# Kernel tuning notes

Measured on AMD Instinct MI355X. Metric: run time of the kernel, lower is better.

The kernel has to match this reference:

```python
import jax, jax.numpy as jnp
import numpy as np

N_NODES = 50000
N_EDGES = 800000
D_IN = 512
D_OUT = 256


def setup_inputs() -> dict:
    key = jax.random.key(0)
    k1, k2, k3 = jax.random.split(key, 3)
    x = jax.random.normal(k1, (N_NODES, D_IN), dtype=jnp.float32)
    edge_index = jax.random.randint(k2, (2, N_EDGES), 0, N_NODES, dtype=jnp.int64)
    # Glorot-style init for the GCN weight, zero bias (PyG defaults)
    W = jax.random.normal(k3, (D_IN, D_OUT), dtype=jnp.float32) * (1.0 / np.sqrt(D_IN))
    b = jnp.zeros((D_OUT,), dtype=jnp.float32)
    return {"x": x, "edge_index": edge_index, "W": W, "b": b}


def reference(x, edge_index, W, b):
    N = x.shape[0]
    # 1) dense linear transform (the compute-heavy GEMM)
    xw = x @ W  # [N, d_out]

    # 2) add self-loops (PyG GCNConv default)
    loop = jnp.arange(N, dtype=edge_index.dtype)
    row = jnp.concatenate([edge_index[0], loop])  # sources
    col = jnp.concatenate([edge_index[1], loop])  # targets

    # 3) symmetric normalization deg^{-1/2} on targets (in-degree incl. self-loops)
    deg = jax.ops.segment_sum(jnp.ones_like(col, dtype=xw.dtype), col, num_segments=N)
    dinv = jnp.where(deg > 0, jax.lax.rsqrt(deg), 0.0)
    norm = dinv[row] * dinv[col]  # [E+N]

    # 4) gather source features, scale, scatter-add to targets
    msgs = xw[row] * norm[:, None]  # [E+N, d_out]
    agg = jax.ops.segment_sum(msgs, col, num_segments=N)  # [N, d_out]

    # 5) bias + ReLU (dropout is identity in eval mode)
    return jax.nn.relu(agg + b)
```

## Files before the change

kernel.cpp:

```cpp
#include <hip/hip_runtime.h>
#include <hip/hip_bf16.h>

#define N_NODES 50000
#define N_EDGES 800000
#define D_IN    512
#define D_OUT   256
#define NBLK_SCAN ((N_NODES + 1023) / 1024)
#define GEMM_NWG (((N_NODES + 127) / 128) * 2)
#define GEMM_Q   (GEMM_NWG / 8)
#define GEMM_R   (GEMM_NWG % 8)
#define FILL_NB  260
#define FUSE_NB  (GEMM_NWG + FILL_NB)
#define GATH_CHUNKS ((N_NODES + 63) / 64)

typedef short s8v  __attribute__((ext_vector_type(8)));
typedef float f32x4 __attribute__((ext_vector_type(4)));

__device__ __forceinline__ unsigned short bf16b(float f) {
    __hip_bfloat16 h = __float2bfloat16(f);
    return *reinterpret_cast<unsigned short*>(&h);
}
__device__ __forceinline__ float bflo(unsigned u) { return __uint_as_float(u << 16); }
__device__ __forceinline__ float bfhi(unsigned u) { return __uint_as_float(u & 0xffff0000u); }

#define GLD16(gp, lp)                                                           \
    __builtin_amdgcn_global_load_lds(                                           \
        (const __attribute__((address_space(1))) unsigned int*)(const void*)(gp),\
        (__attribute__((address_space(3))) unsigned int*)(void*)(lp), 16, 0, 0)

__device__ __forceinline__ int wave_incl_scan(int v, int lane) {
    #pragma unroll
    for (int d = 1; d < 64; d <<= 1) {
        int u = __shfl_up(v, d, 64);
        if (lane >= d) v += u;
    }
    return v;
}

__global__ void k_wt(const float* __restrict__ W, unsigned short* __restrict__ Wt,
                     int* __restrict__ cnt4) {
    int k = blockIdx.x;
    int n = threadIdx.x;
    Wt[(size_t)n * D_IN + k] = bf16b(W[(size_t)k * D_OUT + n]);
    int t = (blockIdx.x * 256 + threadIdx.x) * 2;
    if (t < 4 * N_NODES) {
        cnt4[t] = 0;
        if (t + 1 < 4 * N_NODES) cnt4[t + 1] = 0;
    }
}


__global__ void k_count(const int* __restrict__ col, int* __restrict__ cnt4) {
    int i = (blockIdx.x * 256 + threadIdx.x) * 2;
    if (i < N_EDGES) {
        int2 c = *(const int2*)&col[i];
        atomicAdd(&cnt4[(i & 3) * N_NODES + c.x], 1);
        atomicAdd(&cnt4[((i + 1) & 3) * N_NODES + c.y], 1);
    }
}

__launch_bounds__(256)
__global__ void k_scan1(const int* __restrict__ cnt4, int* __restrict__ bsum) {
    const int t = threadIdx.x, b = blockIdx.x;
    const int idx = b * 1024 + t * 4;
    int s = 0;
    if (idx < N_NODES) {
        #pragma unroll
        for (int q = 0; q < 4; ++q) {
            int4 v = *(const int4*)&cnt4[q * N_NODES + idx];
            s += (v.x + v.y) + (v.z + v.w);
        }
    }
    #pragma unroll
    for (int d = 1; d < 64; d <<= 1) s += __shfl_xor(s, d, 64);
    __shared__ int ws[4];
    if ((t & 63) == 0) ws[t >> 6] = s;
    __syncthreads();
    if (t == 0) bsum[b] = ws[0] + ws[1] + ws[2] + ws[3];
}

__launch_bounds__(256)
__global__ void k_scan3(const int* __restrict__ cnt4, const int* __restrict__ bsum,
                        int* __restrict__ row_ptr, float* __restrict__ dinv,
                        int* __restrict__ cursor4) {
    const int t = threadIdx.x, b = blockIdx.x;
    const int lane = t & 63, wv = t >> 6;
    const int idx = b * 1024 + t * 4;
    int4 vq[4];
    int4 tot = make_int4(0, 0, 0, 0);
    if (idx < N_NODES) {
        #pragma unroll
        for (int q = 0; q < 4; ++q) {
            vq[q] = *(const int4*)&cnt4[q * N_NODES + idx];
            tot.x += vq[q].x; tot.y += vq[q].y;
            tot.z += vq[q].z; tot.w += vq[q].w;
        }
    } else {
        #pragma unroll
        for (int q = 0; q < 4; ++q) vq[q] = make_int4(0, 0, 0, 0);
    }
    int s = (tot.x + tot.y) + (tot.z + tot.w);
    int isc = wave_incl_scan(s, lane);
    __shared__ int wsum[4];
    __shared__ int s_boff;
    if (lane == 63) wsum[wv] = isc;
    if (t < 64) {
        int u = (t < b) ? bsum[t] : 0;
        #pragma unroll
        for (int d = 1; d < 64; d <<= 1) u += __shfl_xor(u, d, 64);
        if (t == 0) s_boff = u;
    }
    __syncthreads();
    int off = s_boff;
    #pragma unroll
    for (int i = 0; i < 4; ++i)
        if (i < wv) off += wsum[i];
    int p0 = off + isc - s;
    int p1 = p0 + tot.x;
    int p2 = p1 + tot.y;
    int p3 = p2 + tot.z;
    if (idx < N_NODES) {
        row_ptr[idx + 0] = p0; dinv[idx + 0] = rsqrtf(1.f + (float)tot.x);
        row_ptr[idx + 1] = p1; dinv[idx + 1] = rsqrtf(1.f + (float)tot.y);
        row_ptr[idx + 2] = p2; dinv[idx + 2] = rsqrtf(1.f + (float)tot.z);
        row_ptr[idx + 3] = p3; dinv[idx + 3] = rsqrtf(1.f + (float)tot.w);
        int4 run = make_int4(p0, p1, p2, p3);
        #pragma unroll
        for (int q = 0; q < 4; ++q) {
            *(int4*)&cursor4[q * N_NODES + idx] = run;
            run.x += vq[q].x; run.y += vq[q].y;
            run.z += vq[q].z; run.w += vq[q].w;
        }
    }
    if (b == 0 && t == 0) row_ptr[N_NODES] = N_EDGES;
}

__launch_bounds__(256)
__global__ void k_gemm(const float* __restrict__ A,
                       const unsigned short* __restrict__ Wt,
                       const float* __restrict__ dinv,
                       unsigned short* __restrict__ yb,
                       const int* __restrict__ row, const int* __restrict__ col,
                       int* __restrict__ cursor4, int* __restrict__ csr_src)
{
    __shared__ __align__(16) float          As[128 * 64];
    __shared__ __align__(16) unsigned short Bs[128 * 64];

    const int bid = blockIdx.x;
    const int t   = threadIdx.x;

    if ((bid & 3) == 3) {
        const int cid = bid >> 2;
        const int stride = FILL_NB * 256 * 2;
        for (int i = (cid * 256 + t) * 2; i < N_EDGES; i += stride) {
            int2 c = *(const int2*)&col[i];
            int2 r = *(const int2*)&row[i];
            int p0 = atomicAdd(&cursor4[(i & 3) * N_NODES + c.x], 1);
            csr_src[p0] = r.x;
            int p1 = atomicAdd(&cursor4[((i + 1) & 3) * N_NODES + c.y], 1);
            csr_src[p1] = r.y;
        }
        return;
    }

    const int gid = bid - (bid >> 2);

    int xcd = gid % 8, pos = gid / 8;
    int wg = (xcd < GEMM_R) ? xcd * (GEMM_Q + 1) + pos
                            : GEMM_R * (GEMM_Q + 1) + (xcd - GEMM_R) * GEMM_Q + pos;
    const int nt = wg & 1;
    const int mt = wg >> 1;
    const int m0 = mt * 128;
    const int n0 = nt * 128;

    const int w  = t >> 6;
    const int l  = t & 63;
    const int wm = (w >> 1) * 64;
    const int wn = (w & 1) * 64;
    const int lr = l & 15;
    const int lk = l >> 4;

    size_t aoff[8];
    #pragma unroll
    for (int i = 0; i < 8; ++i) {
        int rw = m0 + w * 32 + i * 4 + (l >> 4);
        if (rw >= N_NODES) rw = 0;
        int sslot = (l & 15) ^ (rw & 7);
        aoff[i] = (size_t)rw * D_IN + sslot * 4;
    }
    const int srow = l >> 3;
    const int srcj = (l & 7) ^ srow;
    size_t boff[4];
    #pragma unroll
    for (int i = 0; i < 4; ++i) {
        int g = w * 4 + i;
        int bn = n0 + g * 8 + srow;
        boff[i] = (size_t)bn * D_IN + srcj * 8;
    }

    f32x4 acc[4][4] = {};

    for (int kk = 0; kk < D_IN; kk += 64) {
        #pragma unroll
        for (int i = 0; i < 8; ++i)
            GLD16(&A[aoff[i] + kk], (char*)As + (w * 32 + i * 4) * 256);
        #pragma unroll
        for (int i = 0; i < 4; ++i)
            GLD16(&Wt[boff[i] + kk], (char*)Bs + (w * 4 + i) * 1024);
        __syncthreads();

        #pragma unroll
        for (int ks = 0; ks < 2; ++ks) {
            s8v af[4], bfr[4];
            #pragma unroll
            for (int f = 0; f < 4; ++f) {
                int rw = wm + f * 16 + lr;
                int a  = (ks * 4 + lk) * 2;
                int s0 = a ^ (lr & 7);
                int s1 = (a + 1) ^ (lr & 7);
                const char* pr = (const char*)As + rw * 256;
                float4 x0 = *(const float4*)(pr + s0 * 16);
                float4 x1 = *(const float4*)(pr + s1 * 16);
                union { s8v v; unsigned short h[8]; } u;
                u.h[0] = bf16b(x0.x); u.h[1] = bf16b(x0.y);
                u.h[2] = bf16b(x0.z); u.h[3] = bf16b(x0.w);
                u.h[4] = bf16b(x1.x); u.h[5] = bf16b(x1.y);
                u.h[6] = bf16b(x1.z); u.h[7] = bf16b(x1.w);
                af[f] = u.v;
            }
            const int kb = (ks * 64 + lk * 16) ^ ((lr & 7) << 4);
            #pragma unroll
            for (int f = 0; f < 4; ++f)
                bfr[f] = *(const s8v*)((const char*)Bs + ((wn + f * 16 + lr) * 128 + kb));
            #pragma unroll
            for (int fm = 0; fm < 4; ++fm)
                #pragma unroll
                for (int fn = 0; fn < 4; ++fn)
                    acc[fm][fn] = __builtin_amdgcn_mfma_f32_16x16x32_bf16(
                        af[fm], bfr[fn], acc[fm][fn], 0, 0, 0);
        }
        __syncthreads();
    }

    #pragma unroll
    for (int fm = 0; fm < 4; ++fm) {
        #pragma unroll
        for (int j = 0; j < 4; ++j) {
            int rw = m0 + wm + fm * 16 + lk * 4 + j;
            if (rw < N_NODES) {
                float s = dinv[rw];
                #pragma unroll
                for (int fn = 0; fn < 4; ++fn) {
                    int cl = n0 + wn + fn * 16 + lr;
                    size_t off = (size_t)(cl >> 5) * (N_NODES * 32)
                               + (size_t)rw * 32 + (cl & 31);
                    yb[off] = bf16b(acc[fm][fn][j] * s);
                }
            }
        }
    }
}

__device__ __forceinline__ void add8(float* acc, uint4 q) {
    unsigned x;
    x = q.x; acc[0] += bflo(x); acc[1] += bfhi(x);
    x = q.y; acc[2] += bflo(x); acc[3] += bfhi(x);
    x = q.z; acc[4] += bflo(x); acc[5] += bfhi(x);
    x = q.w; acc[6] += bflo(x); acc[7] += bfhi(x);
}

__launch_bounds__(256)
__global__ void k_gather(const int* __restrict__ row_ptr, const int* __restrict__ csr_src,
                         const unsigned short* __restrict__ yb,
                         const float* __restrict__ dinv,
                         const float* __restrict__ bias, float* __restrict__ out)
{
    const int s     = blockIdx.x & 7;
    const int chunk = blockIdx.x >> 3;
    const int g     = threadIdx.x >> 2;
    const int cs    = threadIdx.x & 3;
    const int c     = chunk * 64 + g;
    if (c >= N_NODES) return;

    const uint4* t4 = (const uint4*)(yb + (size_t)s * N_NODES * 32);

    float acc[8] = {0.f,0.f,0.f,0.f,0.f,0.f,0.f,0.f};

    const int e0 = row_ptr[c];
    const int e1 = row_ptr[c + 1];
    for (int i = e0; i < e1; i += 8) {
        int idx[8];
        #pragma unroll
        for (int j = 0; j < 8; ++j) {
            int p = i + j;
            idx[j] = csr_src[p < e1 ? p : e1 - 1];
        }
        uint4 v[8];
        #pragma unroll
        for (int j = 0; j < 8; ++j) v[j] = t4[(size_t)idx[j] * 4 + cs];
        #pragma unroll
        for (int j = 0; j < 8; ++j)
            if (i + j < e1) add8(acc, v[j]);
    }

    add8(acc, t4[(size_t)c * 4 + cs]);

    const float sc = dinv[c];
    const int colb = s * 32 + cs * 8;
    float4 b0 = *(const float4*)&bias[colb];
    float4 b1 = *(const float4*)&bias[colb + 4];
    float4 o0, o1;
    o0.x = fmaxf(fmaf(acc[0], sc, b0.x), 0.f);
    o0.y = fmaxf(fmaf(acc[1], sc, b0.y), 0.f);
    o0.z = fmaxf(fmaf(acc[2], sc, b0.z), 0.f);
    o0.w = fmaxf(fmaf(acc[3], sc, b0.w), 0.f);
    o1.x = fmaxf(fmaf(acc[4], sc, b1.x), 0.f);
    o1.y = fmaxf(fmaf(acc[5], sc, b1.y), 0.f);
    o1.z = fmaxf(fmaf(acc[6], sc, b1.z), 0.f);
    o1.w = fmaxf(fmaf(acc[7], sc, b1.w), 0.f);
    float* dst = &out[(size_t)c * D_OUT + colb];
    *(float4*)dst       = o0;
    *(float4*)(dst + 4) = o1;
}

extern "C" void kernel_launch(void* const* d_in, const int* in_sizes, int n_in,
                              void* d_out, int out_size, void* d_ws, size_t ws_size,
                              hipStream_t stream) {
    const float* x   = (const float*)d_in[0];
    const int*   ei  = (const int*)d_in[1];
    const float* W   = (const float*)d_in[2];
    const float* b   = (const float*)d_in[3];
    float*       out = (float*)d_out;

    const int* row = ei;
    const int* col = ei + N_EDGES;

    char* p = (char*)d_ws;
    unsigned short* yb = (unsigned short*)p;  p += (size_t)N_NODES * D_OUT * 2;
    unsigned short* Wt = (unsigned short*)p;  p += (size_t)D_OUT * D_IN * 2;
    int*   csr_src = (int*)p;                 p += (size_t)N_EDGES * 4;
    int*   cnt4    = (int*)p;                 p += (size_t)4 * N_NODES * 4;
    int*   row_ptr = (int*)p;                 p += (size_t)(N_NODES + 4) * 4;
    int*   cursor4 = (int*)p;                 p += (size_t)4 * N_NODES * 4;
    float* dinv    = (float*)p;               p += (size_t)N_NODES * 4;
    int*   bsum    = (int*)p;                 p += (size_t)NBLK_SCAN * 4;

    k_wt   <<<D_IN, D_OUT, 0, stream>>>(W, Wt, cnt4);
    k_count<<<(N_EDGES / 2 + 255) / 256, 256, 0, stream>>>(col, cnt4);
    k_scan1<<<NBLK_SCAN, 256, 0, stream>>>(cnt4, bsum);
    k_scan3<<<NBLK_SCAN, 256, 0, stream>>>(cnt4, bsum, row_ptr, dinv, cursor4);

    k_gemm<<<FUSE_NB, 256, 0, stream>>>(x, Wt, dinv, yb, row, col, cursor4, csr_src);

    k_gather<<<GATH_CHUNKS * 8, 256, 0, stream>>>(row_ptr, csr_src, yb, dinv, b, out);
}
```

Baseline: 187.7 us.

## Split CSR fill out of GEMM, widen atomic counter banks to eight, merge transpose with count

```diff
diff --git a/kernel.cpp b/kernel.cpp
--- a/kernel.cpp
+++ b/kernel.cpp
@@ -9,9 +9,9 @@
 #define GEMM_NWG (((N_NODES + 127) / 128) * 2)
 #define GEMM_Q   (GEMM_NWG / 8)
 #define GEMM_R   (GEMM_NWG % 8)
-#define FILL_NB  260
-#define FUSE_NB  (GEMM_NWG + FILL_NB)
 #define GATH_CHUNKS ((N_NODES + 63) / 64)
+#define WT_NB    512
+#define CNT_NB   1563
 
 typedef short s8v  __attribute__((ext_vector_type(8)));
 typedef float f32x4 __attribute__((ext_vector_type(4)));
@@ -37,37 +37,34 @@
     return v;
 }
 
-__global__ void k_wt(const float* __restrict__ W, unsigned short* __restrict__ Wt,
-                     int* __restrict__ cnt4) {
-    int k = blockIdx.x;
-    int n = threadIdx.x;
-    Wt[(size_t)n * D_IN + k] = bf16b(W[(size_t)k * D_OUT + n]);
-    int t = (blockIdx.x * 256 + threadIdx.x) * 2;
-    if (t < 4 * N_NODES) {
-        cnt4[t] = 0;
-        if (t + 1 < 4 * N_NODES) cnt4[t + 1] = 0;
-    }
-}
-
-
-__global__ void k_count(const int* __restrict__ col, int* __restrict__ cnt4) {
-    int i = (blockIdx.x * 256 + threadIdx.x) * 2;
+__global__ void k_wtcnt(const float* __restrict__ W, unsigned short* __restrict__ Wt,
+                        const int* __restrict__ col, int* __restrict__ cnt8) {
+    const int bid = blockIdx.x;
+    const int t   = threadIdx.x;
+    if (bid < WT_NB) {
+        int k = bid;
+        int n = t;
+        Wt[(size_t)n * D_IN + k] = bf16b(W[(size_t)k * D_OUT + n]);
+        return;
+    }
+    const int cid = bid - WT_NB;
+    int i = (cid * 256 + t) * 2;
     if (i < N_EDGES) {
         int2 c = *(const int2*)&col[i];
-        atomicAdd(&cnt4[(i & 3) * N_NODES + c.x], 1);
-        atomicAdd(&cnt4[((i + 1) & 3) * N_NODES + c.y], 1);
+        atomicAdd(&cnt8[(i & 7) * N_NODES + c.x], 1);
+        atomicAdd(&cnt8[((i + 1) & 7) * N_NODES + c.y], 1);
     }
 }
 
 __launch_bounds__(256)
-__global__ void k_scan1(const int* __restrict__ cnt4, int* __restrict__ bsum) {
+__global__ void k_scan1(const int* __restrict__ cnt8, int* __restrict__ bsum) {
     const int t = threadIdx.x, b = blockIdx.x;
     const int idx = b * 1024 + t * 4;
     int s = 0;
     if (idx < N_NODES) {
         #pragma unroll
-        for (int q = 0; q < 4; ++q) {
-            int4 v = *(const int4*)&cnt4[q * N_NODES + idx];
+        for (int q = 0; q < 8; ++q) {
+            int4 v = *(const int4*)&cnt8[q * N_NODES + idx];
             s += (v.x + v.y) + (v.z + v.w);
         }
     }
@@ -80,24 +77,24 @@
 }
 
 __launch_bounds__(256)
-__global__ void k_scan3(const int* __restrict__ cnt4, const int* __restrict__ bsum,
+__global__ void k_scan3(const int* __restrict__ cnt8, const int* __restrict__ bsum,
                         int* __restrict__ row_ptr, float* __restrict__ dinv,
-                        int* __restrict__ cursor4) {
+                        int* __restrict__ cursor8) {
     const int t = threadIdx.x, b = blockIdx.x;
     const int lane = t & 63, wv = t >> 6;
     const int idx = b * 1024 + t * 4;
-    int4 vq[4];
+    int4 vq[8];
     int4 tot = make_int4(0, 0, 0, 0);
     if (idx < N_NODES) {
         #pragma unroll
-        for (int q = 0; q < 4; ++q) {
-            vq[q] = *(const int4*)&cnt4[q * N_NODES + idx];
+        for (int q = 0; q < 8; ++q) {
+            vq[q] = *(const int4*)&cnt8[q * N_NODES + idx];
             tot.x += vq[q].x; tot.y += vq[q].y;
             tot.z += vq[q].z; tot.w += vq[q].w;
         }
     } else {
         #pragma unroll
-        for (int q = 0; q < 4; ++q) vq[q] = make_int4(0, 0, 0, 0);
+        for (int q = 0; q < 8; ++q) vq[q] = make_int4(0, 0, 0, 0);
     }
     int s = (tot.x + tot.y) + (tot.z + tot.w);
     int isc = wave_incl_scan(s, lane);
@@ -126,46 +123,39 @@
         row_ptr[idx + 3] = p3; dinv[idx + 3] = rsqrtf(1.f + (float)tot.w);
         int4 run = make_int4(p0, p1, p2, p3);
         #pragma unroll
-        for (int q = 0; q < 4; ++q) {
-            *(int4*)&cursor4[q * N_NODES + idx] = run;
+        for (int q = 0; q < 8; ++q) {
+            *(int4*)&cursor8[q * N_NODES + idx] = run;
             run.x += vq[q].x; run.y += vq[q].y;
             run.z += vq[q].z; run.w += vq[q].w;
         }
     }
     if (b == 0 && t == 0) row_ptr[N_NODES] = N_EDGES;
+}
+
+__global__ void k_fill(const int* __restrict__ row, const int* __restrict__ col,
+                       int* __restrict__ cursor8, int* __restrict__ csr_src) {
+    int i = (blockIdx.x * 256 + threadIdx.x) * 2;
+    if (i < N_EDGES) {
+        int2 c = *(const int2*)&col[i];
+        int2 r = *(const int2*)&row[i];
+        int p0 = atomicAdd(&cursor8[(i & 7) * N_NODES + c.x], 1);
+        csr_src[p0] = r.x;
+        int p1 = atomicAdd(&cursor8[((i + 1) & 7) * N_NODES + c.y], 1);
+        csr_src[p1] = r.y;
+    }
 }
 
 __launch_bounds__(256)
 __global__ void k_gemm(const float* __restrict__ A,
                        const unsigned short* __restrict__ Wt,
                        const float* __restrict__ dinv,
-                       unsigned short* __restrict__ yb,
-                       const int* __restrict__ row, const int* __restrict__ col,
-                       int* __restrict__ cursor4, int* __restrict__ csr_src)
+                       unsigned short* __restrict__ yb)
 {
     __shared__ __align__(16) float          As[128 * 64];
     __shared__ __align__(16) unsigned short Bs[128 * 64];
 
-    const int bid = blockIdx.x;
-    const int t   = threadIdx.x;
-
-    if ((bid & 3) == 3) {
-        const int cid = bid >> 2;
-        const int stride = FILL_NB * 256 * 2;
-        for (int i = (cid * 256 + t) * 2; i < N_EDGES; i += stride) {
-            int2 c = *(const int2*)&col[i];
-            int2 r = *(const int2*)&row[i];
-            int p0 = atomicAdd(&cursor4[(i & 3) * N_NODES + c.x], 1);
-            csr_src[p0] = r.x;
-            int p1 = atomicAdd(&cursor4[((i + 1) & 3) * N_NODES + c.y], 1);
-            csr_src[p1] = r.y;
-        }
-        return;
-    }
-
-    const int gid = bid - (bid >> 2);
-
-    int xcd = gid % 8, pos = gid / 8;
+    int orig = blockIdx.x;
+    int xcd = orig % 8, pos = orig / 8;
     int wg = (xcd < GEMM_R) ? xcd * (GEMM_Q + 1) + pos
                             : GEMM_R * (GEMM_Q + 1) + (xcd - GEMM_R) * GEMM_Q + pos;
     const int nt = wg & 1;
@@ -173,6 +163,7 @@
     const int m0 = mt * 128;
     const int n0 = nt * 128;
 
+    const int t  = threadIdx.x;
     const int w  = t >> 6;
     const int l  = t & 63;
     const int wm = (w >> 1) * 64;
@@ -339,18 +330,19 @@
     unsigned short* yb = (unsigned short*)p;  p += (size_t)N_NODES * D_OUT * 2;
     unsigned short* Wt = (unsigned short*)p;  p += (size_t)D_OUT * D_IN * 2;
     int*   csr_src = (int*)p;                 p += (size_t)N_EDGES * 4;
-    int*   cnt4    = (int*)p;                 p += (size_t)4 * N_NODES * 4;
+    int*   cnt8    = (int*)p;                 p += (size_t)8 * N_NODES * 4;
     int*   row_ptr = (int*)p;                 p += (size_t)(N_NODES + 4) * 4;
-    int*   cursor4 = (int*)p;                 p += (size_t)4 * N_NODES * 4;
+    int*   cursor8 = (int*)p;                 p += (size_t)8 * N_NODES * 4;
     float* dinv    = (float*)p;               p += (size_t)N_NODES * 4;
     int*   bsum    = (int*)p;                 p += (size_t)NBLK_SCAN * 4;
 
-    k_wt   <<<D_IN, D_OUT, 0, stream>>>(W, Wt, cnt4);
-    k_count<<<(N_EDGES / 2 + 255) / 256, 256, 0, stream>>>(col, cnt4);
-    k_scan1<<<NBLK_SCAN, 256, 0, stream>>>(cnt4, bsum);
-    k_scan3<<<NBLK_SCAN, 256, 0, stream>>>(cnt4, bsum, row_ptr, dinv, cursor4);
-
-    k_gemm<<<FUSE_NB, 256, 0, stream>>>(x, Wt, dinv, yb, row, col, cursor4, csr_src);
+    hipMemsetAsync(cnt8, 0, (size_t)8 * N_NODES * sizeof(int), stream);
+    k_wtcnt<<<WT_NB + CNT_NB, 256, 0, stream>>>(W, Wt, col, cnt8);
+    k_scan1<<<NBLK_SCAN, 256, 0, stream>>>(cnt8, bsum);
+    k_scan3<<<NBLK_SCAN, 256, 0, stream>>>(cnt8, bsum, row_ptr, dinv, cursor8);
+    k_fill <<<(N_EDGES / 2 + 255) / 256, 256, 0, stream>>>(row, col, cursor8, csr_src);
+
+    k_gemm<<<GEMM_NWG, 256, 0, stream>>>(x, Wt, dinv, yb);
 
     k_gather<<<GATH_CHUNKS * 8, 256, 0, stream>>>(row_ptr, csr_src, yb, dinv, b, out);
 }
```

Result: no change. 187.8 us (+0.1%).
